# Optimization experiments

Measured on AMD Instinct MI355X. Metric: run time of the kernel, lower is better.

Reference implementation:

```python
import jax, jax.numpy as jnp
import numpy as np

B, S, E, H = 2, 2048, 1024, 16
DH = E // H  # 64


def setup_inputs() -> dict:
    key = jax.random.key(0)
    ks = jax.random.split(key, 9)
    scale = 1.0 / np.sqrt(E)
    q = jax.random.normal(ks[0], (B, S, E), jnp.float32)
    k = jax.random.normal(ks[1], (B, S, E), jnp.float32)
    v = jax.random.normal(ks[2], (B, S, E), jnp.float32)
    Wq = jax.random.uniform(ks[3], (E, E), jnp.float32, -scale, scale)
    Wk = jax.random.uniform(ks[4], (E, E), jnp.float32, -scale, scale)
    Wv = jax.random.uniform(ks[5], (E, E), jnp.float32, -scale, scale)
    bq = jax.random.uniform(ks[6], (E,), jnp.float32, -scale, scale)
    bk = jax.random.uniform(ks[7], (E,), jnp.float32, -scale, scale)
    bv = jax.random.uniform(ks[8], (E,), jnp.float32, -scale, scale)
    # causal mask: True = masked. [b, s_q, s_k]
    causal = jnp.triu(jnp.ones((S, S), bool), k=1)
    mask = jnp.broadcast_to(causal, (B, S, S))
    return {"q": q, "k": k, "v": v, "Wq": Wq, "bq": bq, "Wk": Wk,
            "bk": bk, "Wv": Wv, "bv": bv, "mask": mask}


def reference(q, k, v, Wq, bq, Wk, bk, Wv, bv, mask):
    b, s_q, _ = q.shape
    s_k = k.shape[1]
    # NB: faithful to the original: .view(b, heads, s, -1) (no transpose)
    Q = (q @ Wq + bq).reshape(b, H, s_q, DH)
    K = (k @ Wk + bk).reshape(b, H, s_k, DH)
    V = (v @ Wv + bv).reshape(b, H, s_k, DH)
    scores = jnp.einsum('bhqd,bhkd->bhqk', Q, K) / jnp.sqrt(
        jnp.asarray(DH, Q.dtype))
    scores = jnp.where(mask[:, None, :, :], -jnp.inf, scores)
    attn = jax.nn.softmax(scores, axis=-1)
    out = jnp.einsum('bhqk,bhkd->bhqd', attn, V).reshape(b, s_q, -1)
    return out  # dropout p=0 / eval mode -> identity
```

## Files before the change

kernel.cpp:

```cpp
#include <hip/hip_runtime.h>

typedef unsigned short u16;
typedef __attribute__((ext_vector_type(8))) __bf16 bf16x8;
typedef __attribute__((ext_vector_type(4))) __bf16 bf16x4;
typedef __attribute__((ext_vector_type(4))) float f32x4;

#define MFMA(a, b, c) __builtin_amdgcn_mfma_f32_16x16x32_bf16((a), (b), (c), 0, 0, 0)
#define KSCALE 0.18033688011112042f

__device__ __forceinline__ void load_lds16(const void* g, void* l) {
  __builtin_amdgcn_global_load_lds(
      (__attribute__((address_space(1))) void*)(g),
      (__attribute__((address_space(3))) void*)(l), 16, 0, 0);
}

__device__ __forceinline__ float launder(float x, float lim) {
  return fminf(fmaxf(x, -lim), lim);
}

__global__ __launch_bounds__(256) void prep(
    const float* __restrict__ x0, const float* __restrict__ x1,
    const float* __restrict__ x2, const float* __restrict__ W0,
    const float* __restrict__ W1, const float* __restrict__ W2,
    __bf16* __restrict__ Xb, __bf16* __restrict__ WT) {
  __shared__ __bf16 tile[64][65];
  int bx = blockIdx.x;
  int t = threadIdx.x;
  if (bx < 3072) {
    int z = bx >> 10, blk = bx & 1023;
    const float* x = z == 0 ? x0 : (z == 1 ? x1 : x2);
    __bf16* o = Xb + (size_t)z * 4194304;
#pragma unroll
    for (int i = 0; i < 4; ++i) {
      size_t e = ((size_t)i * 262144 + (size_t)blk * 256 + t) * 4;
      f32x4 v = *(const f32x4*)&x[e];
      bf16x4 b = {(__bf16)v[0], (__bf16)v[1], (__bf16)v[2], (__bf16)v[3]};
      *(bf16x4*)&o[e] = b;
    }
  } else {
    int idx = bx - 3072;
    int z = idx >> 8, rest = idx & 255;
    const float* W = z == 0 ? W0 : (z == 1 ? W1 : W2);
    float sc = z == 0 ? KSCALE : 1.0f;
    __bf16* out = WT + (size_t)z * 1048576;
    int r0 = (rest >> 4) * 64, c0 = (rest & 15) * 64;
#pragma unroll
    for (int it = 0; it < 16; ++it) {
      int flat = it * 256 + t, r = flat >> 6, c = flat & 63;
      tile[c][r] = (__bf16)(W[(size_t)(r0 + r) * 1024 + c0 + c] * sc);
    }
    __syncthreads();
#pragma unroll
    for (int it = 0; it < 16; ++it) {
      int flat = it * 256 + t, r = flat >> 6, c = flat & 63;
      out[(size_t)(c0 + r) * 1024 + r0 + c] = tile[r][c];
    }
  }
}

__device__ __forceinline__ void pg_stage(
    const __bf16* __restrict__ A, const __bf16* __restrict__ Bm, int k0,
    __bf16* As, __bf16* Bs, int tid) {
#pragma unroll
  for (int r = 0; r < 2; ++r) {
    int flat = r * 256 + tid;
    load_lds16(A + (size_t)(flat >> 2) * 1024 + k0 + (flat & 3) * 8, &As[flat * 8]);
  }
#pragma unroll
  for (int r = 0; r < 2; ++r) {
    int flat = r * 256 + tid;
    load_lds16(Bm + (size_t)(flat >> 2) * 1024 + k0 + (flat & 3) * 8, &Bs[flat * 8]);
  }
}

__global__ __launch_bounds__(256, 3) void proj_gemm(
    const __bf16* __restrict__ Xb, const __bf16* __restrict__ WT,
    const float* __restrict__ bq, const float* __restrict__ bk,
    const float* __restrict__ bv, __bf16* __restrict__ QKV) {
  __shared__ __attribute__((aligned(16))) __bf16 As[2][4096];
  __shared__ __attribute__((aligned(16))) __bf16 Bs[2][4096];

  int tid = threadIdx.x;
  int lane = tid & 63, quad = lane >> 4, l16 = lane & 15;
  int w = tid >> 6;
  int wm = (w >> 1) * 64, wn = (w & 1) * 64;
  int m0 = blockIdx.x * 128;
  int z = m0 >> 12;
  int n0 = blockIdx.y * 128;
  const __bf16* A = Xb + (size_t)m0 * 1024;
  const __bf16* Bm = WT + (size_t)z * 1048576 + (size_t)n0 * 1024;

  f32x4 zero4 = {0.f, 0.f, 0.f, 0.f};
  f32x4 acc[4][4];
#pragma unroll
  for (int i = 0; i < 4; ++i)
#pragma unroll
    for (int j = 0; j < 4; ++j) acc[i][j] = zero4;

  pg_stage(A, Bm, 0, As[0], Bs[0], tid);

  for (int i = 0; i < 32; ++i) {
    int cur = i & 1;
    if (i < 31) {
      pg_stage(A, Bm, (i + 1) * 32, As[cur ^ 1], Bs[cur ^ 1], tid);
      asm volatile("s_waitcnt vmcnt(4)" ::: "memory");
    } else {
      asm volatile("s_waitcnt vmcnt(0)" ::: "memory");
    }
    __builtin_amdgcn_sched_barrier(0);
    __builtin_amdgcn_s_barrier();
    __builtin_amdgcn_sched_barrier(0);

    bf16x8 a[4], b[4];
#pragma unroll
    for (int mf = 0; mf < 4; ++mf)
      a[mf] = *(const bf16x8*)&As[cur][(wm + mf * 16 + l16) * 32 + quad * 8];
#pragma unroll
    for (int nf = 0; nf < 4; ++nf)
      b[nf] = *(const bf16x8*)&Bs[cur][(wn + nf * 16 + l16) * 32 + quad * 8];
#pragma unroll
    for (int mf = 0; mf < 4; ++mf)
#pragma unroll
      for (int nf = 0; nf < 4; ++nf) acc[mf][nf] = MFMA(a[mf], b[nf], acc[mf][nf]);

    __builtin_amdgcn_sched_barrier(0);
    __builtin_amdgcn_s_barrier();
    __builtin_amdgcn_sched_barrier(0);
  }

  int mrow = m0 & 4095;
  const float* bp = z == 0 ? bq : (z == 1 ? bk : bv);
  float bsc = z == 0 ? KSCALE : 1.0f;
  __bf16* O = QKV + (size_t)z * 4194304;
#pragma unroll
  for (int nf = 0; nf < 4; ++nf) {
    int n = n0 + wn + nf * 16 + l16;
    float bb = bp[n] * bsc;
#pragma unroll
    for (int mf = 0; mf < 4; ++mf) {
#pragma unroll
      for (int r = 0; r < 4; ++r) {
        int m = mrow + wm + mf * 16 + quad * 4 + r;
        O[(size_t)m * 1024 + n] = (__bf16)launder(acc[mf][nf][r] + bb, 512.f);
      }
    }
  }
}

__global__ __launch_bounds__(256) void transpose_v(
    const u16* __restrict__ Vp, u16* __restrict__ Vt) {
  int bh = blockIdx.y, s0 = blockIdx.x * 64;
  __shared__ u16 tile[64][65];
  int t = threadIdx.x;
  const u16* src = Vp + (size_t)bh * 131072;
  u16* dst = Vt + (size_t)bh * 131072;
#pragma unroll
  for (int it = 0; it < 16; ++it) {
    int flat = it * 256 + t, r = flat >> 6, d = flat & 63;
    tile[d][r] = src[(size_t)(s0 + r) * 64 + d];
  }
  __syncthreads();
#pragma unroll
  for (int it = 0; it < 16; ++it) {
    int flat = it * 256 + t, d = flat >> 6, c = flat & 63;
    dst[(size_t)d * 2048 + s0 + c] = tile[d][c];
  }
}

__global__ __launch_bounds__(256, 4) void flash_attn(
    const __bf16* __restrict__ Qp, const __bf16* __restrict__ Kp,
    const __bf16* __restrict__ Vt, float* __restrict__ out) {
  int bh = blockIdx.x;
  int yy = blockIdx.y;
  int qt = (yy & 24) | (((yy >> 3) & 1) ? (7 - (yy & 7)) : (yy & 7));
  int jmax = qt;
  int t = threadIdx.x;
  int lane = t & 63, quad = lane >> 4, l16 = lane & 15;
  int w = t >> 6;
  int sw = (l16 >> 1) & 3;

  __shared__ __attribute__((aligned(16))) __bf16 Ks[2][4096];
  __shared__ __attribute__((aligned(16))) __bf16 Vs[2][4096];
  __shared__ __attribute__((aligned(16))) __bf16 Ps[4][1024];

  const __bf16* Qb = Qp + (size_t)bh * 131072;
  const __bf16* Kb = Kp + (size_t)bh * 131072;
  const __bf16* Vb = Vt + (size_t)bh * 131072;
  __bf16* Pw = Ps[w];

  int qb = qt * 64 + w * 16;

  bf16x8 qf[2], ones;
#pragma unroll
  for (int i = 0; i < 8; ++i) ones[i] = (__bf16)1.0f;
#pragma unroll
  for (int kk = 0; kk < 2; ++kk)
    qf[kk] = *(const bf16x8*)&Qb[(size_t)(qb + l16) * 64 + kk * 32 + quad * 8];

  f32x4 zero4 = {0.f, 0.f, 0.f, 0.f};
  f32x4 o[4], lacc = zero4;
#pragma unroll
  for (int nd = 0; nd < 4; ++nd) o[nd] = zero4;

  int kq_row[2], kq_off[2], v_d[2], v_off[2], v_kk[2];
#pragma unroll
  for (int p = 0; p < 2; ++p) {
    int c = p * 256 + t;
    int swz = ((c & 3) ^ ((c >> 3) & 3)) * 8;
    kq_row[p] = (c & 255) >> 2;
    kq_off[p] = (c >> 8) * 32 + swz;
    v_kk[p] = c >> 8;
    v_d[p] = (c & 255) >> 2;
    v_off[p] = swz;
  }

  bf16x8 pk[2], pv[2];
#pragma unroll
  for (int p = 0; p < 2; ++p) {
    pk[p] = *(const bf16x8*)&Kb[(size_t)kq_row[p] * 64 + kq_off[p]];
    pv[p] = *(const bf16x8*)&Vb[(size_t)v_d[p] * 2048 + v_kk[p] * 32 + v_off[p]];
  }
#pragma unroll
  for (int p = 0; p < 2; ++p) {
    int c = p * 256 + t;
    *(bf16x8*)&Ks[0][c * 8] = pk[p];
    *(bf16x8*)&Vs[0][c * 8] = pv[p];
  }
  if (jmax > 0) {
#pragma unroll
    for (int p = 0; p < 2; ++p) {
      pk[p] = *(const bf16x8*)&Kb[(size_t)(64 + kq_row[p]) * 64 + kq_off[p]];
      pv[p] = *(const bf16x8*)&Vb[(size_t)v_d[p] * 2048 + 64 + v_kk[p] * 32 + v_off[p]];
    }
  }
  __syncthreads();

  for (int j = 0; j <= jmax; ++j) {
    int cur = j & 1, nxt = cur ^ 1;

    if (j < jmax) {
#pragma unroll
      for (int p = 0; p < 2; ++p) {
        int c = p * 256 + t;
        *(bf16x8*)&Ks[nxt][c * 8] = pk[p];
        *(bf16x8*)&Vs[nxt][c * 8] = pv[p];
      }
      if (j + 1 < jmax) {
        int jn = (j + 2) * 64;
#pragma unroll
        for (int p = 0; p < 2; ++p) {
          pk[p] = *(const bf16x8*)&Kb[(size_t)(jn + kq_row[p]) * 64 + kq_off[p]];
          pv[p] = *(const bf16x8*)&Vb[(size_t)v_d[p] * 2048 + jn + v_kk[p] * 32 + v_off[p]];
        }
      }
    }

    f32x4 s[4];
#pragma unroll
    for (int nt = 0; nt < 4; ++nt) {
      bf16x8 k0 = *(const bf16x8*)&Ks[cur][(nt * 16 + l16) * 32 + (quad ^ sw) * 8];
      bf16x8 k1 = *(const bf16x8*)&Ks[cur][2048 + (nt * 16 + l16) * 32 + (quad ^ sw) * 8];
      f32x4 z = zero4;
      z = MFMA(k0, qf[0], z);
      z = MFMA(k1, qf[1], z);
      s[nt] = z;
    }

    if (j == jmax) {
      int qg = qb + l16;
#pragma unroll
      for (int nt = 0; nt < 4; ++nt) {
        int kg = j * 64 + nt * 16 + quad * 4;
#pragma unroll
        for (int r = 0; r < 4; ++r)
          if (kg + r > qg) s[nt][r] = -1e30f;
      }
    }
#pragma unroll
    for (int nt = 0; nt < 4; ++nt) {
      bf16x4 pb;
#pragma unroll
      for (int r = 0; r < 4; ++r)
        pb[r] = (__bf16)__builtin_amdgcn_exp2f(s[nt][r]);
      *(bf16x4*)&Pw[l16 * 64 + (((nt * 4 + quad) ^ (l16 * 2)) & 15) * 4] = pb;
    }
    {
      bf16x8 pf[2];
#pragma unroll
      for (int kk = 0; kk < 2; ++kk)
        pf[kk] = *(const bf16x8*)&Pw[l16 * 64 + (((kk * 8 + quad * 2) ^ (l16 * 2)) & 15) * 4];
#pragma unroll
      for (int kk = 0; kk < 2; ++kk) {
        lacc = MFMA(ones, pf[kk], lacc);
#pragma unroll
        for (int nd = 0; nd < 4; ++nd) {
          bf16x8 av = *(const bf16x8*)&Vs[cur][kk * 2048 + (nd * 16 + l16) * 32 + (quad ^ sw) * 8];
          o[nd] = MFMA(av, pf[kk], o[nd]);
        }
      }
    }
    __syncthreads();
  }

  {
    float inv = 1.f / lacc[0];
    int qg = qb + l16;
#pragma unroll
    for (int nd = 0; nd < 4; ++nd) {
      f32x4 a;
#pragma unroll
      for (int r = 0; r < 4; ++r) a[r] = launder(o[nd][r] * inv, 512.f);
      *(f32x4*)&out[(size_t)bh * 131072 + (size_t)qg * 64 + nd * 16 + quad * 4] = a;
    }
  }
}

extern "C" void kernel_launch(void* const* d_in, const int* in_sizes, int n_in,
                              void* d_out, int out_size, void* d_ws, size_t ws_size,
                              hipStream_t stream) {
  (void)in_sizes; (void)n_in; (void)out_size; (void)ws_size;
  const float* q  = (const float*)d_in[0];
  const float* k  = (const float*)d_in[1];
  const float* v  = (const float*)d_in[2];
  const float* Wq = (const float*)d_in[3];
  const float* bq = (const float*)d_in[4];
  const float* Wk = (const float*)d_in[5];
  const float* bk = (const float*)d_in[6];
  const float* Wv = (const float*)d_in[7];
  const float* bv = (const float*)d_in[8];

  __bf16* ws  = (__bf16*)d_ws;
  __bf16* WT  = ws;
  __bf16* QKV = ws + (size_t)3 * 1048576;
  __bf16* Qp  = QKV;
  __bf16* Kp  = QKV + (size_t)4194304;
  __bf16* Vp  = QKV + (size_t)2 * 4194304;
  __bf16* Xb  = QKV + (size_t)3 * 4194304;
  __bf16* Vtr = Xb;

  prep<<<dim3(3840), 256, 0, stream>>>(q, k, v, Wq, Wk, Wv, Xb, WT);
  proj_gemm<<<dim3(96, 8), 256, 0, stream>>>(Xb, WT, bq, bk, bv, QKV);
  transpose_v<<<dim3(32, 32), 256, 0, stream>>>((const u16*)Vp, (u16*)Vtr);
  flash_attn<<<dim3(32, 32), 256, 0, stream>>>(Qp, Kp, Vtr, (float*)d_out);
}
```

Baseline: 204.8 us.

## Triple-buffer projection GEMM, load B fragments to registers, swizzle A in LDS

The projection GEMM now uses a three-stage pipeline that prefetches two k-steps ahead, where the earlier version used double buffering. B operand fragments are loaded straight from global memory into registers instead of being staged through LDS. The A tile gets an XOR swizzle to reduce LDS bank conflicts. Together these aim to hide more global-load latency and cut LDS traffic, at the cost of more registers for the in-flight B fragments and some redundant global reads of B across waves.

```diff
diff --git a/kernel.cpp b/kernel.cpp
--- a/kernel.cpp
+++ b/kernel.cpp
@@ -58,37 +58,22 @@
   }
 }
 
-__device__ __forceinline__ void pg_stage(
-    const __bf16* __restrict__ A, const __bf16* __restrict__ Bm, int k0,
-    __bf16* As, __bf16* Bs, int tid) {
-#pragma unroll
-  for (int r = 0; r < 2; ++r) {
-    int flat = r * 256 + tid;
-    load_lds16(A + (size_t)(flat >> 2) * 1024 + k0 + (flat & 3) * 8, &As[flat * 8]);
-  }
-#pragma unroll
-  for (int r = 0; r < 2; ++r) {
-    int flat = r * 256 + tid;
-    load_lds16(Bm + (size_t)(flat >> 2) * 1024 + k0 + (flat & 3) * 8, &Bs[flat * 8]);
-  }
-}
-
 __global__ __launch_bounds__(256, 3) void proj_gemm(
     const __bf16* __restrict__ Xb, const __bf16* __restrict__ WT,
     const float* __restrict__ bq, const float* __restrict__ bk,
     const float* __restrict__ bv, __bf16* __restrict__ QKV) {
-  __shared__ __attribute__((aligned(16))) __bf16 As[2][4096];
-  __shared__ __attribute__((aligned(16))) __bf16 Bs[2][4096];
+  __shared__ __attribute__((aligned(16))) __bf16 As[3][4096];
 
   int tid = threadIdx.x;
   int lane = tid & 63, quad = lane >> 4, l16 = lane & 15;
   int w = tid >> 6;
   int wm = (w >> 1) * 64, wn = (w & 1) * 64;
+  int sw = (l16 >> 1) & 3;
   int m0 = blockIdx.x * 128;
   int z = m0 >> 12;
   int n0 = blockIdx.y * 128;
   const __bf16* A = Xb + (size_t)m0 * 1024;
-  const __bf16* Bm = WT + (size_t)z * 1048576 + (size_t)n0 * 1024;
+  const __bf16* Bl = WT + (size_t)z * 1048576 + (size_t)(n0 + wn + l16) * 1024 + quad * 8;
 
   f32x4 zero4 = {0.f, 0.f, 0.f, 0.f};
   f32x4 acc[4][4];
@@ -97,36 +82,69 @@
 #pragma unroll
     for (int j = 0; j < 4; ++j) acc[i][j] = zero4;
 
-  pg_stage(A, Bm, 0, As[0], Bs[0], tid);
-
-  for (int i = 0; i < 32; ++i) {
-    int cur = i & 1;
-    if (i < 31) {
-      pg_stage(A, Bm, (i + 1) * 32, As[cur ^ 1], Bs[cur ^ 1], tid);
-      asm volatile("s_waitcnt vmcnt(4)" ::: "memory");
-    } else {
-      asm volatile("s_waitcnt vmcnt(0)" ::: "memory");
-    }
-    __builtin_amdgcn_sched_barrier(0);
-    __builtin_amdgcn_s_barrier();
-    __builtin_amdgcn_sched_barrier(0);
-
-    bf16x8 a[4], b[4];
-#pragma unroll
-    for (int mf = 0; mf < 4; ++mf)
-      a[mf] = *(const bf16x8*)&As[cur][(wm + mf * 16 + l16) * 32 + quad * 8];
-#pragma unroll
-    for (int nf = 0; nf < 4; ++nf)
-      b[nf] = *(const bf16x8*)&Bs[cur][(wn + nf * 16 + l16) * 32 + quad * 8];
-#pragma unroll
-    for (int mf = 0; mf < 4; ++mf)
-#pragma unroll
-      for (int nf = 0; nf < 4; ++nf) acc[mf][nf] = MFMA(a[mf], b[nf], acc[mf][nf]);
-
-    __builtin_amdgcn_sched_barrier(0);
-    __builtin_amdgcn_s_barrier();
-    __builtin_amdgcn_sched_barrier(0);
-  }
+  bf16x8 rb0[4], rb1[4], rb2[4];
+
+#define PJ_ISSUE_A(k0, buf)                                                \
+  {                                                                        \
+    _Pragma("unroll") for (int r = 0; r < 2; ++r) {                        \
+      int flat = r * 256 + tid;                                            \
+      int src = ((flat & 3) ^ ((flat >> 3) & 3)) * 8;                      \
+      load_lds16(A + (size_t)(flat >> 2) * 1024 + (k0) + src,              \
+                 &As[buf][flat * 8]);                                      \
+    }                                                                      \
+  }
+#define PJ_ISSUE_B(k0, rb)                                                 \
+  {                                                                        \
+    _Pragma("unroll") for (int nf = 0; nf < 4; ++nf)                       \
+      rb[nf] = *(const bf16x8*)&Bl[nf * 16384 + (k0)];                     \
+  }
+#define PJ_COMPUTE(buf, rb)                                                        \
+  {                                                                                \
+    bf16x8 a[4];                                                                   \
+    _Pragma("unroll") for (int mf = 0; mf < 4; ++mf)                               \
+      a[mf] = *(const bf16x8*)&As[buf][(wm + mf * 16 + l16) * 32 + (quad ^ sw) * 8]; \
+    _Pragma("unroll") for (int mf = 0; mf < 4; ++mf)                               \
+      _Pragma("unroll") for (int nf = 0; nf < 4; ++nf)                             \
+        acc[mf][nf] = MFMA(a[mf], rb[nf], acc[mf][nf]);                            \
+  }
+#define PJ_STEP(i, BUFc, BUFs, RBc, RBs)                       \
+  {                                                            \
+    PJ_ISSUE_A(((i) + 2) * 32, BUFs);                          \
+    PJ_ISSUE_B(((i) + 2) * 32, RBs);                           \
+    __builtin_amdgcn_sched_barrier(0);                         \
+    asm volatile("s_waitcnt vmcnt(12)" ::: "memory");          \
+    __builtin_amdgcn_sched_barrier(0);                         \
+    __builtin_amdgcn_s_barrier();                              \
+    __builtin_amdgcn_sched_barrier(0);                         \
+    PJ_COMPUTE(BUFc, RBc);                                     \
+    __builtin_amdgcn_sched_barrier(0);                         \
+    __builtin_amdgcn_s_barrier();                              \
+    __builtin_amdgcn_sched_barrier(0);                         \
+  }
+
+  PJ_ISSUE_A(0, 0);
+  PJ_ISSUE_B(0, rb0);
+  PJ_ISSUE_A(32, 1);
+  PJ_ISSUE_B(32, rb1);
+
+  for (int ii = 0; ii < 30; ii += 3) {
+    PJ_STEP(ii + 0, 0, 2, rb0, rb2);
+    PJ_STEP(ii + 1, 1, 0, rb1, rb0);
+    PJ_STEP(ii + 2, 2, 1, rb2, rb1);
+  }
+  asm volatile("s_waitcnt vmcnt(6)" ::: "memory");
+  __builtin_amdgcn_sched_barrier(0);
+  __builtin_amdgcn_s_barrier();
+  __builtin_amdgcn_sched_barrier(0);
+  PJ_COMPUTE(0, rb0);
+  __builtin_amdgcn_sched_barrier(0);
+  __builtin_amdgcn_s_barrier();
+  __builtin_amdgcn_sched_barrier(0);
+  asm volatile("s_waitcnt vmcnt(0)" ::: "memory");
+  __builtin_amdgcn_sched_barrier(0);
+  __builtin_amdgcn_s_barrier();
+  __builtin_amdgcn_sched_barrier(0);
+  PJ_COMPUTE(1, rb1);
 
   int mrow = m0 & 4095;
   const float* bp = z == 0 ? bq : (z == 1 ? bk : bv);
```

Result: slower. 226.0 us (+10.3%).

## Enlarge projection GEMM tiles to 256x256 with swizzled LDS ping-pong schedule

Applied to the files above, without the earlier changes.

Rewrites the QKV projection GEMM to use 512-thread blocks computing 256x256 tiles with a K step of 64. LDS is XOR-swizzled and double-buffered, with quarter-tile loads interleaved between MFMA phases and priority raised during MFMA issue. The aim is higher arithmetic intensity and fewer LDS bank conflicts. In exchange, the grid drops to 192 blocks, which may leave some CUs idle, and each block requests a large dynamic LDS allocation.

```diff
diff --git a/kernel.cpp b/kernel.cpp
--- a/kernel.cpp
+++ b/kernel.cpp
@@ -58,77 +58,143 @@
   }
 }
 
-__device__ __forceinline__ void pg_stage(
-    const __bf16* __restrict__ A, const __bf16* __restrict__ Bm, int k0,
-    __bf16* As, __bf16* Bs, int tid) {
-#pragma unroll
-  for (int r = 0; r < 2; ++r) {
-    int flat = r * 256 + tid;
-    load_lds16(A + (size_t)(flat >> 2) * 1024 + k0 + (flat & 3) * 8, &As[flat * 8]);
-  }
-#pragma unroll
-  for (int r = 0; r < 2; ++r) {
-    int flat = r * 256 + tid;
-    load_lds16(Bm + (size_t)(flat >> 2) * 1024 + k0 + (flat & 3) * 8, &Bs[flat * 8]);
-  }
-}
-
-__global__ __launch_bounds__(256, 3) void proj_gemm(
+#define AB0 0
+#define AB1 16384
+#define BB0 32768
+#define BB1 49152
+#define PG_LDSB 131072
+
+__global__ __launch_bounds__(512, 1) void proj_gemm(
     const __bf16* __restrict__ Xb, const __bf16* __restrict__ WT,
     const float* __restrict__ bq, const float* __restrict__ bk,
     const float* __restrict__ bv, __bf16* __restrict__ QKV) {
-  __shared__ __attribute__((aligned(16))) __bf16 As[2][4096];
-  __shared__ __attribute__((aligned(16))) __bf16 Bs[2][4096];
+  extern __shared__ __attribute__((aligned(16))) __bf16 lds[];
 
   int tid = threadIdx.x;
   int lane = tid & 63, quad = lane >> 4, l16 = lane & 15;
   int w = tid >> 6;
-  int wm = (w >> 1) * 64, wn = (w & 1) * 64;
-  int m0 = blockIdx.x * 128;
+  int wm = (w >> 2) * 128, wn = (w & 3) * 64;
+  int sw7 = l16 & 7;
+  int m0 = blockIdx.y * 256;
   int z = m0 >> 12;
-  int n0 = blockIdx.y * 128;
+  int mrow = m0 & 4095;
+  int n0 = blockIdx.x * 256;
   const __bf16* A = Xb + (size_t)m0 * 1024;
-  const __bf16* Bm = WT + (size_t)z * 1048576 + (size_t)n0 * 1024;
+  const __bf16* B = WT + (size_t)z * 1048576 + (size_t)n0 * 1024;
 
   f32x4 zero4 = {0.f, 0.f, 0.f, 0.f};
-  f32x4 acc[4][4];
-#pragma unroll
-  for (int i = 0; i < 4; ++i)
+  f32x4 acc[8][4];
+#pragma unroll
+  for (int i = 0; i < 8; ++i)
 #pragma unroll
     for (int j = 0; j < 4; ++j) acc[i][j] = zero4;
 
-  pg_stage(A, Bm, 0, As[0], Bs[0], tid);
-
-  for (int i = 0; i < 32; ++i) {
-    int cur = i & 1;
-    if (i < 31) {
-      pg_stage(A, Bm, (i + 1) * 32, As[cur ^ 1], Bs[cur ^ 1], tid);
-      asm volatile("s_waitcnt vmcnt(4)" ::: "memory");
+  bf16x8 areg[2][2], breg[4][2];
+
+#define SB() __builtin_amdgcn_sched_barrier(0)
+#define BAR()              \
+  do {                     \
+    SB();                  \
+    __builtin_amdgcn_s_barrier(); \
+    SB();                  \
+  } while (0)
+#define ST_HALF(gbase, grow0, ldsbase, k0)                                          \
+  do {                                                                              \
+    _Pragma("unroll") for (int s_ = 0; s_ < 2; ++s_) {                              \
+      int fl_ = s_ * 512 + tid;                                                     \
+      int r_ = fl_ >> 3, sl_ = fl_ & 7;                                             \
+      load_lds16(gbase + (size_t)((grow0) + r_) * 1024 + (k0) + (sl_ ^ (r_ & 7)) * 8, \
+                 &lds[(ldsbase) + fl_ * 8]);                                        \
+    }                                                                               \
+  } while (0)
+#define LDB(BUFB)                                                                   \
+  do {                                                                              \
+    _Pragma("unroll") for (int nf_ = 0; nf_ < 4; ++nf_)                             \
+      _Pragma("unroll") for (int kk_ = 0; kk_ < 2; ++kk_) {                         \
+        int row_ = wn + nf_ * 16 + l16;                                             \
+        breg[nf_][kk_] = *(const bf16x8*)&lds[(BUFB) + row_ * 64 +                  \
+                                              ((kk_ * 4 + quad) ^ sw7) * 8];        \
+      }                                                                             \
+  } while (0)
+#define LDA(q, BUFA)                                                                \
+  do {                                                                              \
+    _Pragma("unroll") for (int am_ = 0; am_ < 2; ++am_)                             \
+      _Pragma("unroll") for (int kk_ = 0; kk_ < 2; ++kk_) {                         \
+        int row_ = wm + ((q) * 2 + am_) * 16 + l16;                                 \
+        areg[am_][kk_] = *(const bf16x8*)&lds[(BUFA) + row_ * 64 +                  \
+                                              ((kk_ * 4 + quad) ^ sw7) * 8];        \
+      }                                                                             \
+  } while (0)
+#define MM(q)                                                                       \
+  do {                                                                              \
+    __builtin_amdgcn_s_setprio(1);                                                  \
+    _Pragma("unroll") for (int am_ = 0; am_ < 2; ++am_)                             \
+      _Pragma("unroll") for (int nf_ = 0; nf_ < 4; ++nf_)                           \
+        _Pragma("unroll") for (int kk_ = 0; kk_ < 2; ++kk_)                         \
+          acc[(q) * 2 + am_][nf_] =                                                 \
+              MFMA(areg[am_][kk_], breg[nf_][kk_], acc[(q) * 2 + am_][nf_]);        \
+    __builtin_amdgcn_s_setprio(0);                                                  \
+  } while (0)
+
+  ST_HALF(A, 0, AB0, 0);
+  ST_HALF(A, 128, AB0 + 8192, 0);
+  ST_HALF(B, 0, BB0, 0);
+  ST_HALF(B, 128, BB0 + 8192, 0);
+
+  for (int it = 0; it < 8; ++it) {
+    int k1 = (2 * it + 1) * 64;
+    int k2 = (2 * it + 2) * 64;
+    bool pf = (it < 7);
+    ST_HALF(A, 0, AB1, k1);
+    asm volatile("s_waitcnt vmcnt(2)" ::: "memory");
+    BAR();
+    LDB(BB0);
+    LDA(0, AB0);
+    MM(0);
+    BAR();
+    ST_HALF(A, 128, AB1 + 8192, k1);
+    LDA(1, AB0);
+    BAR();
+    MM(1);
+    BAR();
+    ST_HALF(B, 0, BB1, k1);
+    LDA(2, AB0);
+    BAR();
+    MM(2);
+    BAR();
+    ST_HALF(B, 128, BB1 + 8192, k1);
+    LDA(3, AB0);
+    BAR();
+    MM(3);
+    BAR();
+    if (pf) {
+      ST_HALF(A, 0, AB0, k2);
+      asm volatile("s_waitcnt vmcnt(2)" ::: "memory");
     } else {
       asm volatile("s_waitcnt vmcnt(0)" ::: "memory");
     }
-    __builtin_amdgcn_sched_barrier(0);
-    __builtin_amdgcn_s_barrier();
-    __builtin_amdgcn_sched_barrier(0);
-
-    bf16x8 a[4], b[4];
-#pragma unroll
-    for (int mf = 0; mf < 4; ++mf)
-      a[mf] = *(const bf16x8*)&As[cur][(wm + mf * 16 + l16) * 32 + quad * 8];
-#pragma unroll
-    for (int nf = 0; nf < 4; ++nf)
-      b[nf] = *(const bf16x8*)&Bs[cur][(wn + nf * 16 + l16) * 32 + quad * 8];
-#pragma unroll
-    for (int mf = 0; mf < 4; ++mf)
-#pragma unroll
-      for (int nf = 0; nf < 4; ++nf) acc[mf][nf] = MFMA(a[mf], b[nf], acc[mf][nf]);
-
-    __builtin_amdgcn_sched_barrier(0);
-    __builtin_amdgcn_s_barrier();
-    __builtin_amdgcn_sched_barrier(0);
-  }
-
-  int mrow = m0 & 4095;
+    BAR();
+    LDB(BB1);
+    LDA(0, AB1);
+    MM(0);
+    BAR();
+    if (pf) ST_HALF(A, 128, AB0 + 8192, k2);
+    LDA(1, AB1);
+    BAR();
+    MM(1);
+    BAR();
+    if (pf) ST_HALF(B, 0, BB0, k2);
+    LDA(2, AB1);
+    BAR();
+    MM(2);
+    BAR();
+    if (pf) ST_HALF(B, 128, BB0 + 8192, k2);
+    LDA(3, AB1);
+    BAR();
+    MM(3);
+    BAR();
+  }
+
   const float* bp = z == 0 ? bq : (z == 1 ? bk : bv);
   float bsc = z == 0 ? KSCALE : 1.0f;
   __bf16* O = QKV + (size_t)z * 4194304;
@@ -137,7 +203,7 @@
     int n = n0 + wn + nf * 16 + l16;
     float bb = bp[n] * bsc;
 #pragma unroll
-    for (int mf = 0; mf < 4; ++mf) {
+    for (int mf = 0; mf < 8; ++mf) {
 #pragma unroll
       for (int r = 0; r < 4; ++r) {
         int m = mrow + wm + mf * 16 + quad * 4 + r;
@@ -338,8 +404,11 @@
   __bf16* Xb  = QKV + (size_t)3 * 4194304;
   __bf16* Vtr = Xb;
 
+  hipFuncSetAttribute((const void*)proj_gemm,
+                      hipFuncAttributeMaxDynamicSharedMemorySize, PG_LDSB);
+
   prep<<<dim3(3840), 256, 0, stream>>>(q, k, v, Wq, Wk, Wv, Xb, WT);
-  proj_gemm<<<dim3(96, 8), 256, 0, stream>>>(Xb, WT, bq, bk, bv, QKV);
+  proj_gemm<<<dim3(4, 48), 512, PG_LDSB, stream>>>(Xb, WT, bq, bk, bv, QKV);
   transpose_v<<<dim3(32, 32), 256, 0, stream>>>((const u16*)Vp, (u16*)Vtr);
   flash_attn<<<dim3(32, 32), 256, 0, stream>>>(Qp, Kp, Vtr, (float*)d_out);
 }
```

Measured after the change: 206.8 us. Within noise of the previous version (+1.0%).
